# Kernel optimization log

Measured on AMD Instinct MI355X. Metric: run time of the kernel, lower is better.

Reference implementation:

```python
import jax, jax.numpy as jnp
import numpy as np

HID = 1024  # hidden size of the bilinear interaction space

def setup_inputs() -> dict:
    key = jax.random.key(0)
    k1, k2, kw1, kb1, kw2, kwo, kbo = jax.random.split(key, 7)
    B, N1, N2, D1, D2, OUT = 4, 128, 128, 768, 768, 2
    s1 = 1.0 / np.sqrt(D1)
    s2 = 1.0 / np.sqrt(D2)
    so = 1.0 / np.sqrt(HID)
    return {
        "input1": jax.random.normal(k1, (B, N1, D1), dtype=jnp.float32),
        "input2": jax.random.normal(k2, (B, N2, D2), dtype=jnp.float32),
        # torch nn.Linear convention: weight [out, in], y = x @ W.T + b
        "W1": jax.random.uniform(kw1, (HID, D1), jnp.float32, -s1, s1),
        "b1": jax.random.uniform(kb1, (HID,), jnp.float32, -s1, s1),
        "W2": jax.random.uniform(kw2, (HID, D2), jnp.float32, -s2, s2),  # bias=False
        "Wo": jax.random.uniform(kwo, (OUT, HID), jnp.float32, -so, so),
        "bo": jax.random.uniform(kbo, (OUT,), jnp.float32, -so, so),
    }

def reference(input1, input2, W1, b1, W2, Wo, bo):
    # in1: [B, N1, HID], in2: [B, N2, HID]
    in1 = jnp.einsum("bnd,hd->bnh", input1, W1) + b1
    in2 = jnp.einsum("bmd,hd->bmh", input2, W2)
    # broadcast outer-sum -> [B, N1, N2, HID], ReLU, then project to OUT
    h = jax.nn.relu(in1[:, :, None, :] + in2[:, None, :, :])
    return jnp.einsum("bnmh,oh->bnmo", h, Wo) + bo
```

## Files before the change

kernel.cpp:

```cpp
#include <hip/hip_runtime.h>
#include <hip/hip_bf16.h>


typedef __attribute__((ext_vector_type(8))) short s16x8;
typedef __attribute__((ext_vector_type(4))) float f32x4;

#define KP 768
#define BK 64
#define KHALF 384
#define NSTEP (KHALF / BK)

__device__ __forceinline__ void gl_lds16(const void* g, void* l) {
    __builtin_amdgcn_global_load_lds(
        (const __attribute__((address_space(1))) unsigned int*)g,
        (__attribute__((address_space(3))) unsigned int*)l, 16, 0, 0);
}

__global__ __launch_bounds__(256) void prepack(
    const float* __restrict__ in1, const float* __restrict__ in2,
    const float* __restrict__ W1, const float* __restrict__ W2,
    ushort* __restrict__ Abig, ushort* __restrict__ Wbig)
{
    const int gid = blockIdx.x * 256 + threadIdx.x;
    const int src = gid / 196608;
    const int rem = gid % 196608;
    const int row = rem / 192;
    const int k4  = (rem % 192) * 4;
    const float* sp;
    ushort* dst;
    if (src == 0) {
        sp  = (row < 512) ? in1 + (size_t)row * 768 + k4
                          : in2 + (size_t)(row - 512) * 768 + k4;
        dst = Abig + (size_t)row * KP + k4;
    } else {
        sp  = (src == 1 ? W1 : W2) + (size_t)row * 768 + k4;
        dst = Wbig + (size_t)(src - 1) * (1024 * KP) + (size_t)row * KP + k4;
    }
    const float4 x = *(const float4*)sp;
    const float xf[4] = {x.x, x.y, x.z, x.w};
    ushort h[4];
    #pragma unroll
    for (int i = 0; i < 4; ++i) {
        __hip_bfloat16 bh = __float2bfloat16(xf[i]);
        h[i] = *(ushort*)&bh;
    }
    *(ushort4*)dst = make_ushort4(h[0], h[1], h[2], h[3]);
}

__global__ __launch_bounds__(512) void gemm_mfma(
    const ushort* __restrict__ Abig, const ushort* __restrict__ Wbig,
    const float* __restrict__ b1, float* __restrict__ hid)
{
    const int t    = threadIdx.x;
    const int lane = t & 63;
    const int w    = t >> 6;
    const int kh   = w >> 2;
    const int ws   = w & 3;
    const int row0 = blockIdx.y * 64;
    const int col0 = blockIdx.x * 64;

    const char* __restrict__ A = (const char*)(Abig + (size_t)row0 * KP);
    const char* __restrict__ W = (const char*)(Wbig
                                   + (row0 < 512 ? (size_t)0 : (size_t)1024 * KP)
                                   + (size_t)col0 * KP);

    __shared__ ushort lds[2][2][2][4096];

    const int srow = t >> 3;
    const int kbyt = (((t & 7) ^ (srow & 7)) << 4);
    const size_t rowoff = (size_t)srow * (KP * 2);

    const int wr = ws >> 1, wc = ws & 1;
    const int l15 = lane & 15, kg = lane >> 4;
    int aoff[2][2], boff[2][2];
    #pragma unroll
    for (int kk = 0; kk < 2; ++kk)
        #pragma unroll
        for (int f = 0; f < 2; ++f) {
            const int r = wr * 32 + f * 16 + l15;
            const int c = wc * 32 + f * 16 + l15;
            const int sw_ = kk * 64 + kg * 16;
            aoff[kk][f] = r * 128 + (sw_ ^ ((r & 7) << 4));
            boff[kk][f] = c * 128 + (sw_ ^ ((c & 7) << 4));
        }

#define STAGE(buf, ktk) do {                                                   \
        const size_t kby = (size_t)(ktk) * (BK * 2);                           \
        _Pragma("unroll")                                                      \
        for (int p = 0; p < 4; ++p) {                                          \
            const char* src = (p & 1) ? W : A;                                 \
            const size_t off = rowoff + (size_t)(p >> 1) * (KHALF * 2)         \
                               + kby + kbyt;                                   \
            gl_lds16(src + off,                                                \
                     (char*)&lds[buf][p >> 1][p & 1][0] + t * 16);             \
        }                                                                      \
    } while (0)

    const f32x4 zero = {0.f, 0.f, 0.f, 0.f};
    f32x4 acc[2][2] = {{zero, zero}, {zero, zero}};

    STAGE(0, 0);
    int cur = 0;
    for (int kt = 0; kt < NSTEP; ++kt) {
        asm volatile("s_waitcnt vmcnt(0)" ::: "memory");
        __syncthreads();
        if (kt + 1 < NSTEP) STAGE(cur ^ 1, kt + 1);
        const char* __restrict__ ab = (const char*)&lds[cur][kh][0][0];
        const char* __restrict__ wb = (const char*)&lds[cur][kh][1][0];
        #pragma unroll
        for (int kk = 0; kk < 2; ++kk) {
            s16x8 af[2], bf_[2];
            #pragma unroll
            for (int f = 0; f < 2; ++f) {
                af[f]  = *(const s16x8*)(ab + aoff[kk][f]);
                bf_[f] = *(const s16x8*)(wb + boff[kk][f]);
            }
            #pragma unroll
            for (int fr = 0; fr < 2; ++fr)
                #pragma unroll
                for (int fc = 0; fc < 2; ++fc)
                    acc[fr][fc] = __builtin_amdgcn_mfma_f32_16x16x32_bf16(
                        af[fr], bf_[fc], acc[fr][fc], 0, 0, 0);
        }
        cur ^= 1;
    }
#undef STAGE

    __syncthreads();
    float* red = (float*)&lds[0][0][0][0];
    if (kh == 1) {
        #pragma unroll
        for (int fr = 0; fr < 2; ++fr)
            #pragma unroll
            for (int fc = 0; fc < 2; ++fc)
                *(f32x4*)&red[(((ws * 2 + fr) * 2 + fc) * 64 + lane) * 4] =
                    acc[fr][fc];
    }
    __syncthreads();
    if (kh == 0) {
        float bias[2] = {0.f, 0.f};
        if (row0 < 512) {
            bias[0] = b1[col0 + wc * 32 + l15];
            bias[1] = b1[col0 + wc * 32 + 16 + l15];
        }
        #pragma unroll
        for (int fr = 0; fr < 2; ++fr)
            #pragma unroll
            for (int fc = 0; fc < 2; ++fc) {
                const f32x4 o = *(const f32x4*)
                    &red[(((ws * 2 + fr) * 2 + fc) * 64 + lane) * 4];
                #pragma unroll
                for (int i = 0; i < 4; ++i) {
                    const int r = row0 + wr * 32 + fr * 16 + kg * 4 + i;
                    const int c = col0 + wc * 32 + fc * 16 + l15;
                    hid[(size_t)r * 1024 + c] = acc[fr][fc][i] + o[i] + bias[fc];
                }
            }
    }
}

__global__ __launch_bounds__(256) void out_init(
    const float* __restrict__ bo, float* __restrict__ out)
{
    const int g = blockIdx.x * 256 + threadIdx.x;
    *(float2*)&out[(size_t)g * 2] = make_float2(bo[0], bo[1]);
}

__global__ __launch_bounds__(256) void pair_kernel(
    const float* __restrict__ hid, const float* __restrict__ Wo,
    float* __restrict__ out)
{
    const int t  = threadIdx.x;
    const int b  = blockIdx.z >> 2;
    const int h0 = (blockIdx.z & 3) * 256;
    const int n0 = blockIdx.y * 16;
    const int m0 = blockIdx.x * 16;

    __shared__ float s1[16][260];
    __shared__ float s2[16][260];
    __shared__ float sw[2][256];

    const float* __restrict__ base1 = hid + ((size_t)(b * 128 + n0)) * 1024 + h0;
    const float* __restrict__ base2 = hid + ((size_t)(512 + b * 128 + m0)) * 1024 + h0;

    #pragma unroll
    for (int p = 0; p < 4; ++p) {
        const int slot = p * 256 + t;
        const int r  = slot >> 6;
        const int c  = (slot & 63) << 2;
        *(float4*)&s1[r][c] = *(const float4*)&base1[(size_t)r * 1024 + c];
        *(float4*)&s2[r][c] = *(const float4*)&base2[(size_t)r * 1024 + c];
    }
    if (t < 128) {
        const int o = t >> 6;
        const int c = (t & 63) << 2;
        *(float4*)&sw[o][c] = *(const float4*)&Wo[(size_t)o * 1024 + h0 + c];
    }
    __syncthreads();

    const int i = t >> 4, j = t & 15;
    const float* __restrict__ xrow = &s1[i][0];
    const float* __restrict__ yrow = &s2[j][0];
    float acc0 = 0.f, acc1 = 0.f;

    #pragma unroll 8
    for (int c4 = 0; c4 < 64; ++c4) {
        const float4 x  = *(const float4*)&xrow[c4 * 4];
        const float4 y  = *(const float4*)&yrow[c4 * 4];
        const float4 uu = *(const float4*)&sw[0][c4 * 4];
        const float4 vv = *(const float4*)&sw[1][c4 * 4];
        float r;
        r = fmaxf(x.x + y.x, 0.f); acc0 = fmaf(r, uu.x, acc0); acc1 = fmaf(r, vv.x, acc1);
        r = fmaxf(x.y + y.y, 0.f); acc0 = fmaf(r, uu.y, acc0); acc1 = fmaf(r, vv.y, acc1);
        r = fmaxf(x.z + y.z, 0.f); acc0 = fmaf(r, uu.z, acc0); acc1 = fmaf(r, vv.z, acc1);
        r = fmaxf(x.w + y.w, 0.f); acc0 = fmaf(r, uu.w, acc0); acc1 = fmaf(r, vv.w, acc1);
    }

    const size_t P = (((size_t)b * 128 + n0 + i) * 128 + (m0 + j)) * 2;
    atomicAdd(&out[P],     acc0);
    atomicAdd(&out[P + 1], acc1);
}

extern "C" void kernel_launch(void* const* d_in, const int* in_sizes, int n_in,
                              void* d_out, int out_size, void* d_ws, size_t ws_size,
                              hipStream_t stream) {
    (void)in_sizes; (void)n_in; (void)out_size; (void)ws_size;
    const float* input1 = (const float*)d_in[0];
    const float* input2 = (const float*)d_in[1];
    const float* W1     = (const float*)d_in[2];
    const float* b1     = (const float*)d_in[3];
    const float* W2     = (const float*)d_in[4];
    const float* Wo     = (const float*)d_in[5];
    const float* bo     = (const float*)d_in[6];
    float* out = (float*)d_out;

    ushort* Abig = (ushort*)d_ws;
    ushort* Wbig = Abig + (size_t)1024 * KP;
    float*  hid  = (float*)(Wbig + (size_t)2 * 1024 * KP);

    prepack<<<2304, 256, 0, stream>>>(input1, input2, W1, W2, Abig, Wbig);
    gemm_mfma<<<dim3(16, 16), 512, 0, stream>>>(Abig, Wbig, b1, hid);
    out_init<<<256, 256, 0, stream>>>(bo, out);
    pair_kernel<<<dim3(8, 8, 16), 256, 0, stream>>>(hid, Wo, out);
}
```

Baseline: 95.11 us.

## Fuse bf16 conversion and output init into GEMM kernel, drop prepack pass

Removes the separate prepack and out_init kernels. The GEMM now loads fp32 inputs and weights through registers, converts them to bf16 and writes them into LDS, and also writes the bias into the output buffer. This saves two kernel launches and the round trip through global memory for the bf16 copies. In exchange, the async global-to-LDS loads become register-staged loads with an extra barrier per step, and each fp32 element is read by every block that uses it, so global read traffic rises.

```diff
diff --git a/kernel.cpp b/kernel.cpp
--- a/kernel.cpp
+++ b/kernel.cpp
@@ -3,6 +3,7 @@
 
 
 typedef __attribute__((ext_vector_type(8))) short s16x8;
+typedef __attribute__((ext_vector_type(8))) unsigned short u16x8;
 typedef __attribute__((ext_vector_type(4))) float f32x4;
 
 #define KP 768
@@ -10,46 +11,22 @@
 #define KHALF 384
 #define NSTEP (KHALF / BK)
 
-__device__ __forceinline__ void gl_lds16(const void* g, void* l) {
-    __builtin_amdgcn_global_load_lds(
-        (const __attribute__((address_space(1))) unsigned int*)g,
-        (__attribute__((address_space(3))) unsigned int*)l, 16, 0, 0);
-}
-
-__global__ __launch_bounds__(256) void prepack(
+__device__ __forceinline__ u16x8 cvt8_bf16(float4 a, float4 b) {
+    const float f[8] = {a.x, a.y, a.z, a.w, b.x, b.y, b.z, b.w};
+    u16x8 r;
+    #pragma unroll
+    for (int i = 0; i < 8; ++i) {
+        __hip_bfloat16 h = __float2bfloat16(f[i]);
+        r[i] = *(unsigned short*)&h;
+    }
+    return r;
+}
+
+__global__ __launch_bounds__(512) void gemm_mfma(
     const float* __restrict__ in1, const float* __restrict__ in2,
     const float* __restrict__ W1, const float* __restrict__ W2,
-    ushort* __restrict__ Abig, ushort* __restrict__ Wbig)
-{
-    const int gid = blockIdx.x * 256 + threadIdx.x;
-    const int src = gid / 196608;
-    const int rem = gid % 196608;
-    const int row = rem / 192;
-    const int k4  = (rem % 192) * 4;
-    const float* sp;
-    ushort* dst;
-    if (src == 0) {
-        sp  = (row < 512) ? in1 + (size_t)row * 768 + k4
-                          : in2 + (size_t)(row - 512) * 768 + k4;
-        dst = Abig + (size_t)row * KP + k4;
-    } else {
-        sp  = (src == 1 ? W1 : W2) + (size_t)row * 768 + k4;
-        dst = Wbig + (size_t)(src - 1) * (1024 * KP) + (size_t)row * KP + k4;
-    }
-    const float4 x = *(const float4*)sp;
-    const float xf[4] = {x.x, x.y, x.z, x.w};
-    ushort h[4];
-    #pragma unroll
-    for (int i = 0; i < 4; ++i) {
-        __hip_bfloat16 bh = __float2bfloat16(xf[i]);
-        h[i] = *(ushort*)&bh;
-    }
-    *(ushort4*)dst = make_ushort4(h[0], h[1], h[2], h[3]);
-}
-
-__global__ __launch_bounds__(512) void gemm_mfma(
-    const ushort* __restrict__ Abig, const ushort* __restrict__ Wbig,
-    const float* __restrict__ b1, float* __restrict__ hid)
+    const float* __restrict__ b1, const float* __restrict__ bo,
+    float* __restrict__ hid, float* __restrict__ out)
 {
     const int t    = threadIdx.x;
     const int lane = t & 63;
@@ -59,16 +36,20 @@
     const int row0 = blockIdx.y * 64;
     const int col0 = blockIdx.x * 64;
 
-    const char* __restrict__ A = (const char*)(Abig + (size_t)row0 * KP);
-    const char* __restrict__ W = (const char*)(Wbig
-                                   + (row0 < 512 ? (size_t)0 : (size_t)1024 * KP)
-                                   + (size_t)col0 * KP);
+    const int gid = (blockIdx.y * 16 + blockIdx.x) * 512 + t;
+    if (gid < 65536) {
+        *(float2*)&out[(size_t)gid * 2] = make_float2(bo[0], bo[1]);
+    }
+
+    const bool first = (row0 < 512);
+    const float* __restrict__ Asrc = first ? in1 + (size_t)row0 * 768
+                                           : in2 + (size_t)(row0 - 512) * 768;
+    const float* __restrict__ Wsrc = (first ? W1 : W2) + (size_t)col0 * 768;
 
     __shared__ ushort lds[2][2][2][4096];
 
-    const int srow = t >> 3;
-    const int kbyt = (((t & 7) ^ (srow & 7)) << 4);
-    const size_t rowoff = (size_t)srow * (KP * 2);
+    const int srow   = t >> 3;
+    const int lchunk = (t & 7) ^ (srow & 7);
 
     const int wr = ws >> 1, wc = ws & 1;
     const int l15 = lane & 15, kg = lane >> 4;
@@ -84,27 +65,30 @@
             boff[kk][f] = c * 128 + (sw_ ^ ((c & 7) << 4));
         }
 
-#define STAGE(buf, ktk) do {                                                   \
-        const size_t kby = (size_t)(ktk) * (BK * 2);                           \
+    float4 ra[4][2];
+#define LOADREGS(ktk) do {                                                     \
         _Pragma("unroll")                                                      \
         for (int p = 0; p < 4; ++p) {                                          \
-            const char* src = (p & 1) ? W : A;                                 \
-            const size_t off = rowoff + (size_t)(p >> 1) * (KHALF * 2)         \
-                               + kby + kbyt;                                   \
-            gl_lds16(src + off,                                                \
-                     (char*)&lds[buf][p >> 1][p & 1][0] + t * 16);             \
+            const float* s = (p & 1) ? Wsrc : Asrc;                            \
+            const size_t off = (size_t)srow * 768 + (p >> 1) * KHALF           \
+                               + (ktk) * BK + lchunk * 8;                      \
+            ra[p][0] = *(const float4*)(s + off);                              \
+            ra[p][1] = *(const float4*)(s + off + 4);                          \
         }                                                                      \
     } while (0)
 
     const f32x4 zero = {0.f, 0.f, 0.f, 0.f};
     f32x4 acc[2][2] = {{zero, zero}, {zero, zero}};
 
-    STAGE(0, 0);
+    LOADREGS(0);
     int cur = 0;
     for (int kt = 0; kt < NSTEP; ++kt) {
-        asm volatile("s_waitcnt vmcnt(0)" ::: "memory");
+        #pragma unroll
+        for (int p = 0; p < 4; ++p)
+            *(u16x8*)((char*)&lds[cur][p >> 1][p & 1][0] + t * 16) =
+                cvt8_bf16(ra[p][0], ra[p][1]);
         __syncthreads();
-        if (kt + 1 < NSTEP) STAGE(cur ^ 1, kt + 1);
+        if (kt + 1 < NSTEP) LOADREGS(kt + 1);
         const char* __restrict__ ab = (const char*)&lds[cur][kh][0][0];
         const char* __restrict__ wb = (const char*)&lds[cur][kh][1][0];
         #pragma unroll
@@ -122,11 +106,11 @@
                     acc[fr][fc] = __builtin_amdgcn_mfma_f32_16x16x32_bf16(
                         af[fr], bf_[fc], acc[fr][fc], 0, 0, 0);
         }
+        __syncthreads();
         cur ^= 1;
     }
-#undef STAGE
-
-    __syncthreads();
+#undef LOADREGS
+
     float* red = (float*)&lds[0][0][0][0];
     if (kh == 1) {
         #pragma unroll
@@ -139,7 +123,7 @@
     __syncthreads();
     if (kh == 0) {
         float bias[2] = {0.f, 0.f};
-        if (row0 < 512) {
+        if (first) {
             bias[0] = b1[col0 + wc * 32 + l15];
             bias[1] = b1[col0 + wc * 32 + 16 + l15];
         }
@@ -157,13 +141,6 @@
                 }
             }
     }
-}
-
-__global__ __launch_bounds__(256) void out_init(
-    const float* __restrict__ bo, float* __restrict__ out)
-{
-    const int g = blockIdx.x * 256 + threadIdx.x;
-    *(float2*)&out[(size_t)g * 2] = make_float2(bo[0], bo[1]);
 }
 
 __global__ __launch_bounds__(256) void pair_kernel(
@@ -233,13 +210,9 @@
     const float* Wo     = (const float*)d_in[5];
     const float* bo     = (const float*)d_in[6];
     float* out = (float*)d_out;
-
-    ushort* Abig = (ushort*)d_ws;
-    ushort* Wbig = Abig + (size_t)1024 * KP;
-    float*  hid  = (float*)(Wbig + (size_t)2 * 1024 * KP);
-
-    prepack<<<2304, 256, 0, stream>>>(input1, input2, W1, W2, Abig, Wbig);
-    gemm_mfma<<<dim3(16, 16), 512, 0, stream>>>(Abig, Wbig, b1, hid);
-    out_init<<<256, 256, 0, stream>>>(bo, out);
+    float* hid = (float*)d_ws;
+
+    gemm_mfma<<<dim3(16, 16), 512, 0, stream>>>(input1, input2, W1, W2,
+                                                b1, bo, hid, out);
     pair_kernel<<<dim3(8, 8, 16), 256, 0, stream>>>(hid, Wo, out);
 }
```

After: 95.34 us. No clear change (+0.2%).
